# Performance work log

Hardware: AMD Instinct MI355X
Metric: run time of the kernel (lower is better)

Reference implementation:

```python
import jax, jax.numpy as jnp
import numpy as np

N = 100000      # nodes
E = 1600000     # edges
H = 128         # hidden_dim
L = 4           # num_layers (blocks AND inner GGC steps)
G = 512         # graphs in batch
IN = 128        # input_dim
OUT = 16        # output_dim
HS = H // 2     # mlp hidden


def setup_inputs() -> dict:
    key = jax.random.key(0)
    ks = jax.random.split(key, 24)
    s = 0.05
    inp = {
        "node_embed": jax.random.normal(ks[0], (N, IN), dtype=jnp.float32),
        "edge_index": jax.random.randint(ks[1], (2, E), 0, N, dtype=jnp.int32),
        "batch": jnp.sort(jax.random.randint(ks[2], (N,), 0, G, dtype=jnp.int32)),
        # nodeEmbed Linear
        "node_w": jax.random.normal(ks[3], (H, IN), dtype=jnp.float32) * s,
        "node_b": jnp.zeros((H,), dtype=jnp.float32),
        # per-block GatedGraphConv weights: [blocks, steps, H, H]
        "ggc_weight": jax.random.normal(ks[4], (L, L, H, H), dtype=jnp.float32) * s,
        # per-block GRUCell weights (torch layout: [3H, H], gates r,z,n)
        "gru_w_ih": jax.random.normal(ks[5], (L, 3 * H, H), dtype=jnp.float32) * s,
        "gru_w_hh": jax.random.normal(ks[6], (L, 3 * H, H), dtype=jnp.float32) * s,
        "gru_b_ih": jnp.zeros((L, 3 * H), dtype=jnp.float32),
        "gru_b_hh": jnp.zeros((L, 3 * H), dtype=jnp.float32),
        # cat_linear: H*L -> H
        "cat_w": jax.random.normal(ks[7], (H, H * L), dtype=jnp.float32) * s,
        "cat_b": jnp.zeros((H,), dtype=jnp.float32),
        # gate_nn: H -> 1
        "gate_w": jax.random.normal(ks[8], (1, H), dtype=jnp.float32) * s,
        "gate_b": jnp.zeros((1,), dtype=jnp.float32),
        # mlp
        "mlp_w1": jax.random.normal(ks[9], (HS, H), dtype=jnp.float32) * s,
        "mlp_b1": jnp.zeros((HS,), dtype=jnp.float32),
        "mlp_w2": jax.random.normal(ks[10], (HS, HS), dtype=jnp.float32) * s,
        "mlp_b2": jnp.zeros((HS,), dtype=jnp.float32),
        # heads
        "out_w": jax.random.normal(ks[11], (OUT, HS), dtype=jnp.float32) * s,
        "out_b": jnp.zeros((OUT,), dtype=jnp.float32),
        "line_w": jax.random.normal(ks[12], (OUT, H), dtype=jnp.float32) * s,
        "line_b": jnp.zeros((OUT,), dtype=jnp.float32),
    }
    return inp


def _gru_cell(m, h, w_ih, w_hh, b_ih, b_hh):
    gi = m @ w_ih.T + b_ih            # [N, 3H]
    gh = h @ w_hh.T + b_hh            # [N, 3H]
    i_r, i_z, i_n = jnp.split(gi, 3, axis=-1)
    h_r, h_z, h_n = jnp.split(gh, 3, axis=-1)
    r = jax.nn.sigmoid(i_r + h_r)
    z = jax.nn.sigmoid(i_z + h_z)
    n = jnp.tanh(i_n + r * h_n)
    return (1.0 - z) * n + z * h


def _gated_graph_conv(x, src, dst, W, w_ih, w_hh, b_ih, b_hh):
    n = x.shape[0]
    for i in range(W.shape[0]):       # fixed small step count
        m = x @ W[i]                  # [N, H]
        agg = jax.ops.segment_sum(m[src], dst, num_segments=n)  # scatter-add messages
        x = _gru_cell(agg, x, w_ih, w_hh, b_ih, b_hh)
    return x


def reference(node_embed, edge_index, batch, node_w, node_b, ggc_weight,
              gru_w_ih, gru_w_hh, gru_b_ih, gru_b_hh, cat_w, cat_b,
              gate_w, gate_b, mlp_w1, mlp_b1, mlp_w2, mlp_b2,
              out_w, out_b, line_w, line_b):
    src, dst = edge_index[0], edge_index[1]
    h0 = node_embed @ node_w.T + node_b                     # nodeEmbed
    # all residual blocks consume the SAME h0 (per original forward loop)
    outs = [
        _gated_graph_conv(h0, src, dst, ggc_weight[k], gru_w_ih[k],
                          gru_w_hh[k], gru_b_ih[k], gru_b_hh[k]) + h0
        for k in range(ggc_weight.shape[0])
    ]
    hidden = jnp.concatenate(outs, axis=-1) @ cat_w.T + cat_b  # [N, H]
    lineout = hidden @ line_w.T + line_b                       # [N, OUT]
    # attentional aggregation: scatter softmax over per-graph gates
    gate = (hidden @ gate_w.T + gate_b)[:, 0]                  # [N]
    gmax = jax.ops.segment_max(gate, batch, num_segments=G)
    ex = jnp.exp(gate - gmax[batch])
    denom = jax.ops.segment_sum(ex, batch, num_segments=G)
    alpha = ex / denom[batch]
    pooled = jax.ops.segment_sum(alpha[:, None] * hidden, batch, num_segments=G)  # [G, H]
    h = jax.nn.relu(pooled @ mlp_w1.T + mlp_b1)
    h = jax.nn.relu(h @ mlp_w2.T + mlp_b2)
    out = h @ out_w.T + out_b                                  # [G, OUT]
    return (out, lineout)
```

## Files before the change

kernel.cpp:

```cpp
#include <hip/hip_runtime.h>

#define N_NODES 100000
#define N_EDGES 1600000
#define HD 128
#define NH (N_NODES * HD)

typedef __attribute__((ext_vector_type(8))) short bf16x8;
typedef __attribute__((ext_vector_type(4))) float f32x4;

__device__ inline unsigned short f2bf(float f) {
  unsigned u = __float_as_uint(f);
  unsigned r = (u + 0x7FFFu + ((u >> 16) & 1u)) >> 16;
  return (unsigned short)r;
}
__device__ inline float bf2f(unsigned short b) {
  return __uint_as_float(((unsigned)b) << 16);
}
__device__ inline float sigm_f(float x) {
  return __builtin_amdgcn_rcpf(1.f + __expf(-x));
}
__device__ inline float tanh_f(float x) {
  return 1.f - 2.f * __builtin_amdgcn_rcpf(__expf(2.f * x) + 1.f);
}

__global__ __launch_bounds__(256) void gemm_h0_k(
    const float* __restrict__ A, const float* __restrict__ B,
    const float* __restrict__ bias, unsigned short* __restrict__ Cb, int M) {
  __shared__ float As[16][132];
  __shared__ float Bs[16][68];
  const int tid = threadIdx.x;
  const int row0 = blockIdx.x * 128;
  const int col0 = blockIdx.y * 64;
  const int tx = tid & 15, ty = tid >> 4;

  float acc[8][4];
#pragma unroll
  for (int i = 0; i < 8; i++)
#pragma unroll
    for (int j = 0; j < 4; j++) acc[i][j] = 0.f;

  const int lr = tid >> 2;
  const int kg = (tid & 3) * 4;

  for (int k0 = 0; k0 < 128; k0 += 16) {
#pragma unroll
    for (int h = 0; h < 2; ++h) {
      int r = lr + h * 64;
      float4 v = make_float4(0.f, 0.f, 0.f, 0.f);
      if (row0 + r < M)
        v = *reinterpret_cast<const float4*>(A + (size_t)(row0 + r) * 128 + k0 + kg);
      As[kg + 0][r] = v.x;
      As[kg + 1][r] = v.y;
      As[kg + 2][r] = v.z;
      As[kg + 3][r] = v.w;
    }
    {
      int c = lr;
      float4 v = *reinterpret_cast<const float4*>(B + (size_t)(col0 + c) * 128 + k0 + kg);
      Bs[kg + 0][c] = v.x;
      Bs[kg + 1][c] = v.y;
      Bs[kg + 2][c] = v.z;
      Bs[kg + 3][c] = v.w;
    }
    __syncthreads();
#pragma unroll
    for (int kk = 0; kk < 16; ++kk) {
      float a[8], b[4];
#pragma unroll
      for (int i = 0; i < 8; i++) a[i] = As[kk][ty * 8 + i];
#pragma unroll
      for (int j = 0; j < 4; j++) b[j] = Bs[kk][tx * 4 + j];
#pragma unroll
      for (int i = 0; i < 8; i++)
#pragma unroll
        for (int j = 0; j < 4; j++) acc[i][j] += a[i] * b[j];
    }
    __syncthreads();
  }

#pragma unroll
  for (int i = 0; i < 8; i++) {
    int r = row0 + ty * 8 + i;
    if (r < M) {
#pragma unroll
      for (int j = 0; j < 4; j++) {
        int c = col0 + tx * 4 + j;
        Cb[(size_t)r * 128 + c] = f2bf(acc[i][j] + bias[c]);
      }
    }
  }
}

__global__ __launch_bounds__(256) void gemm_wct_k(
    const float* __restrict__ w_ih, const float* __restrict__ ggc_w,
    float* __restrict__ Cout) {
  const int z = blockIdx.z;
  const float* A = w_ih + (size_t)(z >> 2) * 384 * 128;
  const float* B = ggc_w + (size_t)z * 128 * 128;
  float* C = Cout + (size_t)z * 384 * 128;
  __shared__ float As[16][132];
  __shared__ float Bs[16][68];
  const int tid = threadIdx.x;
  const int row0 = blockIdx.x * 128;
  const int col0 = blockIdx.y * 64;
  const int tx = tid & 15, ty = tid >> 4;

  float acc[8][4];
#pragma unroll
  for (int i = 0; i < 8; i++)
#pragma unroll
    for (int j = 0; j < 4; j++) acc[i][j] = 0.f;

  const int lr = tid >> 2;
  const int kg = (tid & 3) * 4;

  for (int k0 = 0; k0 < 128; k0 += 16) {
#pragma unroll
    for (int h = 0; h < 2; ++h) {
      int r = lr + h * 64;
      float4 v = *reinterpret_cast<const float4*>(A + (size_t)(row0 + r) * 128 + k0 + kg);
      As[kg + 0][r] = v.x;
      As[kg + 1][r] = v.y;
      As[kg + 2][r] = v.z;
      As[kg + 3][r] = v.w;
    }
    {
      int c = lr;
      float4 v = *reinterpret_cast<const float4*>(B + (size_t)(col0 + c) * 128 + k0 + kg);
      Bs[kg + 0][c] = v.x;
      Bs[kg + 1][c] = v.y;
      Bs[kg + 2][c] = v.z;
      Bs[kg + 3][c] = v.w;
    }
    __syncthreads();
#pragma unroll
    for (int kk = 0; kk < 16; ++kk) {
      float a[8], b[4];
#pragma unroll
      for (int i = 0; i < 8; i++) a[i] = As[kk][ty * 8 + i];
#pragma unroll
      for (int j = 0; j < 4; j++) b[j] = Bs[kk][tx * 4 + j];
#pragma unroll
      for (int i = 0; i < 8; i++)
#pragma unroll
        for (int j = 0; j < 4; j++) acc[i][j] += a[i] * b[j];
    }
    __syncthreads();
  }

#pragma unroll
  for (int i = 0; i < 8; i++) {
    int r = row0 + ty * 8 + i;
#pragma unroll
    for (int j = 0; j < 4; j++) {
      int c = col0 + tx * 4 + j;
      C[(size_t)r * 128 + c] = acc[i][j];
    }
  }
}

__global__ __launch_bounds__(256) void f2b_k(const float* __restrict__ a,
                                             unsigned short* __restrict__ b, int n) {
  int i = blockIdx.x * 256 + threadIdx.x;
  if (i * 4 >= n) return;
  float4 v = reinterpret_cast<const float4*>(a)[i];
  ushort4 o;
  o.x = f2bf(v.x);
  o.y = f2bf(v.y);
  o.z = f2bf(v.z);
  o.w = f2bf(v.w);
  reinterpret_cast<ushort4*>(b)[i] = o;
}

template <bool LAST>
__global__ __launch_bounds__(256) void gru_mfma4_k(
    const unsigned short* __restrict__ aggb,
    const unsigned short* __restrict__ xb_base, size_t xstride,
    const unsigned short* __restrict__ h0b,
    const unsigned short* __restrict__ wct_base, size_t wct_zs,
    const unsigned short* __restrict__ whh_base, size_t whh_zs,
    const float* __restrict__ bih_base, const float* __restrict__ bhh_base,
    unsigned short* __restrict__ xbout,
    int M, int nRowTiles) {
  const int z = blockIdx.z;
  const unsigned short* agg = aggb + (size_t)z * NH;
  const unsigned short* xb = xb_base + (size_t)z * xstride;
  unsigned short* out = xbout + (size_t)z * NH;
  const unsigned short* wctb = wct_base + (size_t)z * wct_zs;
  const unsigned short* whhb = whh_base + (size_t)z * whh_zs;
  const float* b_ih = bih_base + z * 384;
  const float* b_hh = bhh_base + z * 384;

  const int lane = threadIdx.x & 63;
  const int wave = threadIdx.x >> 6;
  const int lrow = lane & 15;
  const int kblk = lane >> 4;
  const int c = blockIdx.y * 16 + lrow;

  bf16x8 wf[6][4];
#pragma unroll
  for (int s = 0; s < 3; s++)
#pragma unroll
    for (int kk = 0; kk < 4; kk++) {
      size_t off = (size_t)(s * 128 + c) * 128 + kk * 32 + kblk * 8;
      wf[s][kk] = *reinterpret_cast<const bf16x8*>(wctb + off);
      wf[s + 3][kk] = *reinterpret_cast<const bf16x8*>(whhb + off);
    }
  const float bi0 = b_ih[c], bi1 = b_ih[128 + c], bi2 = b_ih[256 + c];
  const float bh0 = b_hh[c], bh1 = b_hh[128 + c], bh2 = b_hh[256 + c];

  const int tstride = gridDim.x * 4;
  for (int rt = blockIdx.x * 4 + wave; rt < nRowTiles; rt += tstride) {
    const int row0 = rt * 16;
    int arow = row0 + lrow;
    if (arow >= M) arow = M - 1;
    const size_t abase = (size_t)arow * 128 + kblk * 8;

    f32x4 acc[6];
#pragma unroll
    for (int s = 0; s < 6; s++) acc[s] = (f32x4)(0.f);
#pragma unroll
    for (int kk = 0; kk < 4; kk++) {
      bf16x8 a_ag = *reinterpret_cast<const bf16x8*>(agg + abase + kk * 32);
      bf16x8 a_x = *reinterpret_cast<const bf16x8*>(xb + abase + kk * 32);
      acc[0] = __builtin_amdgcn_mfma_f32_16x16x32_bf16(a_ag, wf[0][kk], acc[0], 0, 0, 0);
      acc[1] = __builtin_amdgcn_mfma_f32_16x16x32_bf16(a_ag, wf[1][kk], acc[1], 0, 0, 0);
      acc[2] = __builtin_amdgcn_mfma_f32_16x16x32_bf16(a_ag, wf[2][kk], acc[2], 0, 0, 0);
      acc[3] = __builtin_amdgcn_mfma_f32_16x16x32_bf16(a_x, wf[3][kk], acc[3], 0, 0, 0);
      acc[4] = __builtin_amdgcn_mfma_f32_16x16x32_bf16(a_x, wf[4][kk], acc[4], 0, 0, 0);
      acc[5] = __builtin_amdgcn_mfma_f32_16x16x32_bf16(a_x, wf[5][kk], acc[5], 0, 0, 0);
    }
#pragma unroll
    for (int r = 0; r < 4; r++) {
      int orow = row0 + kblk * 4 + r;
      if (orow >= M) continue;
      size_t idx = (size_t)orow * 128 + c;
      float ir = acc[0][r] + bi0;
      float iz = acc[1][r] + bi1;
      float in_ = acc[2][r] + bi2;
      float hr = acc[3][r] + bh0;
      float hz = acc[4][r] + bh1;
      float hn = acc[5][r] + bh2;
      float rg = sigm_f(ir + hr);
      float zg = sigm_f(iz + hz);
      float ng = tanh_f(in_ + rg * hn);
      float h = bf2f(xb[idx]);
      float nv = (1.f - zg) * ng + zg * h;
      if (LAST) nv += bf2f(h0b[idx]);
      out[idx] = f2bf(nv);
    }
  }
}

__global__ __launch_bounds__(256) void cat_mfma2_k(
    const unsigned short* __restrict__ outs,
    const unsigned short* __restrict__ wcatb,
    const float* __restrict__ cat_b, float* __restrict__ hidden, int M, int pair) {
  const int lane = threadIdx.x & 63;
  const int wave = threadIdx.x >> 6;
  const int row0 = blockIdx.x * 64 + wave * 16;
  const int c0 = blockIdx.y * 32;
  const int lrow = lane & 15;
  const int kb = lane >> 4;
  int arow = row0 + lrow;
  if (arow >= M) arow = M - 1;

  f32x4 acc[2];
  acc[0] = (f32x4)(0.f);
  acc[1] = (f32x4)(0.f);
#pragma unroll
  for (int kk = 0; kk < 8; kk++) {
    const unsigned short* ob = outs + (size_t)(kk >> 2) * NH;
    bf16x8 a = *reinterpret_cast<const bf16x8*>(
        ob + (size_t)arow * 128 + (kk & 3) * 32 + kb * 8);
#pragma unroll
    for (int t = 0; t < 2; t++) {
      bf16x8 b = *reinterpret_cast<const bf16x8*>(
          wcatb + (size_t)(c0 + t * 16 + lrow) * 512 + pair * 256 + (kk >> 2) * 128 +
          (kk & 3) * 32 + kb * 8);
      acc[t] = __builtin_amdgcn_mfma_f32_16x16x32_bf16(a, b, acc[t], 0, 0, 0);
    }
  }
#pragma unroll
  for (int r = 0; r < 4; r++) {
    int orow = row0 + kb * 4 + r;
    if (orow >= M) continue;
#pragma unroll
    for (int t = 0; t < 2; t++) {
      int c = c0 + t * 16 + lrow;
      size_t idx = (size_t)orow * 128 + c;
      float v = acc[t][r];
      v += (pair == 0) ? cat_b[c] : hidden[idx];
      hidden[idx] = v;
    }
  }
}

__global__ __launch_bounds__(256) void deg_hist_k(const int* __restrict__ dst,
                                                  int* __restrict__ deg) {
  int e = blockIdx.x * 256 + threadIdx.x;
  if (e >= N_EDGES) return;
  atomicAdd(&deg[dst[e]], 1);
}

__global__ __launch_bounds__(256) void scan1_k(const int* __restrict__ deg,
                                               int* __restrict__ offsets,
                                               int* __restrict__ bsum) {
  __shared__ int buf[256];
  int tid = threadIdx.x;
  int idx = blockIdx.x * 256 + tid;
  int v = (idx < N_NODES) ? deg[idx] : 0;
  buf[tid] = v;
  __syncthreads();
  for (int off = 1; off < 256; off <<= 1) {
    int t = (tid >= off) ? buf[tid - off] : 0;
    __syncthreads();
    buf[tid] += t;
    __syncthreads();
  }
  if (idx < N_NODES) offsets[idx] = buf[tid] - v;
  if (tid == 255) bsum[blockIdx.x] = buf[255];
}

__global__ __launch_bounds__(512) void scan2_k(int* __restrict__ bsum, int nb) {
  __shared__ int buf[512];
  int tid = threadIdx.x;
  int v = (tid < nb) ? bsum[tid] : 0;
  buf[tid] = v;
  __syncthreads();
  for (int off = 1; off < 512; off <<= 1) {
    int t = (tid >= off) ? buf[tid - off] : 0;
    __syncthreads();
    buf[tid] += t;
    __syncthreads();
  }
  if (tid < nb) bsum[tid] = buf[tid] - v;
}

__global__ __launch_bounds__(256) void scan3_k(int* __restrict__ offsets,
                                               const int* __restrict__ bsum) {
  int idx = blockIdx.x * 256 + threadIdx.x;
  if (idx < N_NODES) offsets[idx] += bsum[idx >> 8];
  if (idx == 0) offsets[N_NODES] = N_EDGES;
}

__global__ __launch_bounds__(256) void copy_int_k(const int* __restrict__ a,
                                                  int* __restrict__ b, int n) {
  int i = blockIdx.x * 256 + threadIdx.x;
  if (i < n) b[i] = a[i];
}

__global__ __launch_bounds__(256) void fill_k(const int* __restrict__ src,
                                              const int* __restrict__ dst,
                                              int* __restrict__ cursor,
                                              int* __restrict__ srcs_sorted) {
  int e = blockIdx.x * 256 + threadIdx.x;
  if (e >= N_EDGES) return;
  int pos = atomicAdd(&cursor[dst[e]], 1);
  srcs_sorted[pos] = src[e];
}

__global__ __launch_bounds__(256) void gather4_k(
    const unsigned short* __restrict__ xb_base, size_t xstride,
    const int* __restrict__ offsets, const int* __restrict__ srcs,
    unsigned short* __restrict__ aggb) {
  int wid = (blockIdx.x * 256 + threadIdx.x) >> 6;
  int lane = threadIdx.x & 63;
  if (wid >= 2 * N_NODES) return;
  int z = (wid >= N_NODES) ? 1 : 0;
  int node = wid - z * N_NODES;
  const unsigned short* xb = xb_base + (size_t)z * xstride;
  int beg = offsets[node], end = offsets[node + 1];
  int half = lane >> 5;
  int cg = (lane & 31) * 4;
  float a0 = 0.f, a1 = 0.f, a2 = 0.f, a3 = 0.f;
  int e = beg + half;
  for (; e + 2 < end; e += 4) {
    int s0 = srcs[e], s1 = srcs[e + 2];
    uint2 v0 = *reinterpret_cast<const uint2*>(xb + (size_t)s0 * 128 + cg);
    uint2 v1 = *reinterpret_cast<const uint2*>(xb + (size_t)s1 * 128 + cg);
    a0 += bf2f((unsigned short)(v0.x & 0xFFFFu));
    a1 += bf2f((unsigned short)(v0.x >> 16));
    a2 += bf2f((unsigned short)(v0.y & 0xFFFFu));
    a3 += bf2f((unsigned short)(v0.y >> 16));
    a0 += bf2f((unsigned short)(v1.x & 0xFFFFu));
    a1 += bf2f((unsigned short)(v1.x >> 16));
    a2 += bf2f((unsigned short)(v1.y & 0xFFFFu));
    a3 += bf2f((unsigned short)(v1.y >> 16));
  }
  if (e < end) {
    int s0 = srcs[e];
    uint2 v0 = *reinterpret_cast<const uint2*>(xb + (size_t)s0 * 128 + cg);
    a0 += bf2f((unsigned short)(v0.x & 0xFFFFu));
    a1 += bf2f((unsigned short)(v0.x >> 16));
    a2 += bf2f((unsigned short)(v0.y & 0xFFFFu));
    a3 += bf2f((unsigned short)(v0.y >> 16));
  }
  a0 += __shfl_down(a0, 32);
  a1 += __shfl_down(a1, 32);
  a2 += __shfl_down(a2, 32);
  a3 += __shfl_down(a3, 32);
  if (half == 0) {
    uint2 o;
    o.x = (unsigned)f2bf(a0) | ((unsigned)f2bf(a1) << 16);
    o.y = (unsigned)f2bf(a2) | ((unsigned)f2bf(a3) << 16);
    *reinterpret_cast<uint2*>(aggb + (size_t)z * NH + (size_t)node * 128 + cg) = o;
  }
}

__global__ __launch_bounds__(256) void lineout_k(
    const float* __restrict__ hidden, const float* __restrict__ W,
    const float* __restrict__ b, float* __restrict__ out) {
  __shared__ float Ws[16 * 128];
  for (int i = threadIdx.x; i < 2048; i += 256) Ws[i] = W[i];
  __syncthreads();
  int r = threadIdx.x >> 4, c = threadIdx.x & 15;
  int n = blockIdx.x * 16 + r;
  if (n >= N_NODES) return;
  const float* h = hidden + (size_t)n * 128;
  const float* w = Ws + c * 128;
  float acc = 0.f;
#pragma unroll 8
  for (int k = 0; k < 128; k++) acc += h[k] * w[k];
  out[(size_t)n * 16 + c] = acc + b[c];
}

__global__ __launch_bounds__(256) void gate_k(
    const float* __restrict__ hidden, const float* __restrict__ gw,
    const float* __restrict__ gb, float* __restrict__ gate) {
  int wid = (blockIdx.x * 256 + threadIdx.x) >> 6;
  int lane = threadIdx.x & 63;
  if (wid >= N_NODES) return;
  const float* h = hidden + (size_t)wid * 128;
  float s = h[lane] * gw[lane] + h[64 + lane] * gw[64 + lane];
#pragma unroll
  for (int off = 32; off; off >>= 1) s += __shfl_down(s, off);
  if (lane == 0) gate[wid] = s + gb[0];
}

__global__ void graph_start_k(const int* __restrict__ batch, int* __restrict__ gs) {
  int g = threadIdx.x;
  if (g > 512) return;
  if (g == 512) {
    gs[512] = N_NODES;
    return;
  }
  int lo = 0, hi = N_NODES;
  while (lo < hi) {
    int mid = (lo + hi) >> 1;
    if (batch[mid] < g) lo = mid + 1;
    else hi = mid;
  }
  gs[g] = lo;
}

__global__ __launch_bounds__(256) void pool_fused_k(
    const float* __restrict__ hidden, const float* __restrict__ gate,
    const int* __restrict__ gs, float* __restrict__ ex,
    float* __restrict__ pooled) {
  const int g = blockIdx.x;
  const int beg = gs[g], end = gs[g + 1];
  const int tid = threadIdx.x, lane = tid & 63, wv = tid >> 6;
  __shared__ float red[4];
  __shared__ float sval;
  __shared__ float colbuf[256];

  if (end <= beg) {
    if (tid < 128) pooled[(size_t)g * 128 + tid] = 0.f;
    return;
  }
  float m = -3.4e38f;
  for (int n = beg + tid; n < end; n += 256) m = fmaxf(m, gate[n]);
#pragma unroll
  for (int off = 32; off; off >>= 1) m = fmaxf(m, __shfl_down(m, off));
  if (lane == 0) red[wv] = m;
  __syncthreads();
  if (tid == 0) sval = fmaxf(fmaxf(red[0], red[1]), fmaxf(red[2], red[3]));
  __syncthreads();
  const float mx = sval;
  float s = 0.f;
  for (int n = beg + tid; n < end; n += 256) {
    float e = __expf(gate[n] - mx);
    ex[n] = e;
    s += e;
  }
#pragma unroll
  for (int off = 32; off; off >>= 1) s += __shfl_down(s, off);
  if (lane == 0) red[wv] = s;
  __syncthreads();
  if (tid == 0) sval = red[0] + red[1] + red[2] + red[3];
  __syncthreads();
  const float denom = sval;
  const int col = tid & 127, half = tid >> 7;
  float acc = 0.f;
  for (int n = beg + half; n < end; n += 2)
    acc += ex[n] * hidden[(size_t)n * 128 + col];
  colbuf[tid] = acc;
  __syncthreads();
  if (tid < 128)
    pooled[(size_t)g * 128 + tid] = (colbuf[tid] + colbuf[tid + 128]) / denom;
}

__global__ void mlp1_k(const float* __restrict__ pooled, const float* __restrict__ w,
                       const float* __restrict__ b, float* __restrict__ h1) {
  int g = blockIdx.x, j = threadIdx.x;
  const float* p = pooled + (size_t)g * 128;
  const float* wr = w + (size_t)j * 128;
  float acc = 0.f;
#pragma unroll 8
  for (int k = 0; k < 128; k++) acc += p[k] * wr[k];
  acc += b[j];
  h1[g * 64 + j] = acc > 0.f ? acc : 0.f;
}

__global__ void mlp2_k(const float* __restrict__ h1, const float* __restrict__ w,
                       const float* __restrict__ b, float* __restrict__ h2) {
  int g = blockIdx.x, j = threadIdx.x;
  const float* p = h1 + (size_t)g * 64;
  const float* wr = w + (size_t)j * 64;
  float acc = 0.f;
#pragma unroll 8
  for (int k = 0; k < 64; k++) acc += p[k] * wr[k];
  acc += b[j];
  h2[g * 64 + j] = acc > 0.f ? acc : 0.f;
}

__global__ void outhead_k(const float* __restrict__ h2, const float* __restrict__ w,
                          const float* __restrict__ b, float* __restrict__ out) {
  int g = blockIdx.x, j = threadIdx.x;
  if (j >= 16) return;
  const float* p = h2 + (size_t)g * 64;
  const float* wr = w + (size_t)j * 64;
  float acc = 0.f;
#pragma unroll 8
  for (int k = 0; k < 64; k++) acc += p[k] * wr[k];
  out[g * 16 + j] = acc + b[j];
}

extern "C" void kernel_launch(void* const* d_in, const int* in_sizes, int n_in,
                              void* d_out, int out_size, void* d_ws, size_t ws_size,
                              hipStream_t stream) {
  const float* node_embed = (const float*)d_in[0];
  const int* eidx = (const int*)d_in[1];
  const int* batch = (const int*)d_in[2];
  const float* node_w = (const float*)d_in[3];
  const float* node_b = (const float*)d_in[4];
  const float* ggc_w = (const float*)d_in[5];
  const float* w_ih = (const float*)d_in[6];
  const float* w_hh = (const float*)d_in[7];
  const float* b_ih = (const float*)d_in[8];
  const float* b_hh = (const float*)d_in[9];
  const float* cat_w = (const float*)d_in[10];
  const float* cat_b = (const float*)d_in[11];
  const float* gate_w = (const float*)d_in[12];
  const float* gate_b = (const float*)d_in[13];
  const float* mlp_w1 = (const float*)d_in[14];
  const float* mlp_b1 = (const float*)d_in[15];
  const float* mlp_w2 = (const float*)d_in[16];
  const float* mlp_b2 = (const float*)d_in[17];
  const float* out_w = (const float*)d_in[18];
  const float* out_b = (const float*)d_in[19];
  const float* line_w = (const float*)d_in[20];
  const float* line_b = (const float*)d_in[21];

  const int* src = eidx;
  const int* dst = eidx + N_EDGES;

  float* hidden = (float*)d_ws;
  unsigned short* h0b = (unsigned short*)(hidden + (size_t)NH);
  unsigned short* X0 = h0b + (size_t)NH;
  unsigned short* X1 = X0 + (size_t)2 * NH;
  unsigned short* aggb = X1 + (size_t)2 * NH;
  unsigned short* wctb = aggb + (size_t)2 * NH;
  unsigned short* whhb = wctb + 16 * 384 * 128;
  unsigned short* wcatb = whhb + 4 * 384 * 128;
  int* offsets = (int*)(wcatb + 128 * 512);
  int* cursor = offsets + N_NODES + 1;
  int* srcs_sorted = cursor + N_NODES;
  int* bsum = srcs_sorted + N_EDGES;
  int* gs = bsum + 512;
  float* WcTf = (float*)aggb;

  float* out_graph = (float*)d_out;
  float* out_line = (float*)d_out + 512 * 16;

  dim3 blk(256);
  const int gM128 = (N_NODES + 127) / 128;
  const int gM64 = (N_NODES + 63) / 64;
  const int gE = (N_EDGES + 255) / 256;
  const int nScanBlk = (N_NODES + 255) / 256;
  const int nRowTiles = (N_NODES + 15) / 16;
  const size_t S = (size_t)384 * 128;

  hipMemsetAsync(cursor, 0, N_NODES * sizeof(int), stream);
  deg_hist_k<<<gE, blk, 0, stream>>>(dst, cursor);
  scan1_k<<<nScanBlk, blk, 0, stream>>>(cursor, offsets, bsum);
  scan2_k<<<1, 512, 0, stream>>>(bsum, nScanBlk);
  scan3_k<<<nScanBlk, blk, 0, stream>>>(offsets, bsum);
  copy_int_k<<<(N_NODES + 255) / 256, blk, 0, stream>>>(offsets, cursor, N_NODES);
  fill_k<<<gE, blk, 0, stream>>>(src, dst, cursor, srcs_sorted);
  graph_start_k<<<1, 576, 0, stream>>>(batch, gs);

  gemm_wct_k<<<dim3(3, 2, 16), blk, 0, stream>>>(w_ih, ggc_w, WcTf);
  f2b_k<<<(16 * 384 * 128 / 4 + 255) / 256, blk, 0, stream>>>(WcTf, wctb, 16 * 384 * 128);
  f2b_k<<<(4 * 384 * 128 / 4 + 255) / 256, blk, 0, stream>>>(w_hh, whhb, 4 * 384 * 128);
  f2b_k<<<(128 * 512 / 4 + 255) / 256, blk, 0, stream>>>(cat_w, wcatb, 128 * 512);

  gemm_h0_k<<<dim3(gM128, 2), blk, 0, stream>>>(node_embed, node_w, node_b, h0b, N_NODES);

  const int gGather = (2 * N_NODES * 64 + 255) / 256;
  const dim3 gruGrid(200, 8, 2);
  for (int p = 0; p < 2; p++) {
    const float* bih_p = b_ih + (size_t)p * 2 * 384;
    const float* bhh_p = b_hh + (size_t)p * 2 * 384;
    const unsigned short* whh_p = whhb + (size_t)p * 2 * S;
    for (int i = 0; i < 4; i++) {
      const unsigned short* wct_pi = wctb + ((size_t)8 * p + i) * S;
      const unsigned short* xin;
      size_t xs;
      unsigned short* xout;
      if (i == 0) { xin = h0b; xs = 0; xout = X0; }
      else if (i == 1) { xin = X0; xs = NH; xout = X1; }
      else if (i == 2) { xin = X1; xs = NH; xout = X0; }
      else { xin = X0; xs = NH; xout = X1; }
      gather4_k<<<gGather, blk, 0, stream>>>(xin, xs, offsets, srcs_sorted, aggb);
      if (i < 3)
        gru_mfma4_k<false><<<gruGrid, blk, 0, stream>>>(
            aggb, xin, xs, h0b, wct_pi, 4 * S, whh_p, S, bih_p, bhh_p, xout,
            N_NODES, nRowTiles);
      else
        gru_mfma4_k<true><<<gruGrid, blk, 0, stream>>>(
            aggb, xin, xs, h0b, wct_pi, 4 * S, whh_p, S, bih_p, bhh_p, xout,
            N_NODES, nRowTiles);
    }
    cat_mfma2_k<<<dim3(gM64, 4), blk, 0, stream>>>(X1, wcatb, cat_b, hidden, N_NODES, p);
  }

  lineout_k<<<(N_NODES + 15) / 16, blk, 0, stream>>>(hidden, line_w, line_b, out_line);

  float* gate = (float*)X0;
  float* ex = (float*)X0 + N_NODES;
  float* pooled = (float*)aggb;
  float* h1 = pooled + 512 * 128;
  float* h2 = h1 + 512 * 64;

  gate_k<<<(N_NODES * 64 + 255) / 256, blk, 0, stream>>>(hidden, gate_w, gate_b, gate);
  pool_fused_k<<<512, blk, 0, stream>>>(hidden, gate, gs, ex, pooled);
  mlp1_k<<<512, 64, 0, stream>>>(pooled, mlp_w1, mlp_b1, h1);
  mlp2_k<<<512, 64, 0, stream>>>(h1, mlp_w2, mlp_b2, h2);
  outhead_k<<<512, 64, 0, stream>>>(h2, out_w, out_b, out_graph);
}
```

Baseline: 2.845 ms.

## Dedupe first-step gather, deepen gather unroll, prefetch GRU epilogue loads, widen grid

At the first GGC step both blocks of a pair read the same h0, so the gather now runs for one block only and both GRU blocks read that single aggregate through a zero z-stride. The gather loop is unrolled to four neighbours per half-wave to keep more loads in flight. The GRU kernel loads the h and h0 epilogue values before the MFMA loop, drops row bounds checks because N is divisible by 16, and doubles the grid x dimension. This removes redundant gather traffic and exposes load latency to overlap, at the cost of relying on N being a multiple of 16.

```diff
diff --git a/kernel.cpp b/kernel.cpp
--- a/kernel.cpp
+++ b/kernel.cpp
@@ -173,17 +173,16 @@
 }
 
 template <bool LAST>
-__global__ __launch_bounds__(256) void gru_mfma4_k(
-    const unsigned short* __restrict__ aggb,
+__global__ __launch_bounds__(256) void gru_mfma5_k(
+    const unsigned short* __restrict__ agg_base, size_t agg_zs,
     const unsigned short* __restrict__ xb_base, size_t xstride,
     const unsigned short* __restrict__ h0b,
     const unsigned short* __restrict__ wct_base, size_t wct_zs,
     const unsigned short* __restrict__ whh_base, size_t whh_zs,
     const float* __restrict__ bih_base, const float* __restrict__ bhh_base,
-    unsigned short* __restrict__ xbout,
-    int M, int nRowTiles) {
+    unsigned short* __restrict__ xbout, int nRowTiles) {
   const int z = blockIdx.z;
-  const unsigned short* agg = aggb + (size_t)z * NH;
+  const unsigned short* agg = agg_base + (size_t)z * agg_zs;
   const unsigned short* xb = xb_base + (size_t)z * xstride;
   unsigned short* out = xbout + (size_t)z * NH;
   const unsigned short* wctb = wct_base + (size_t)z * wct_zs;
@@ -212,9 +211,15 @@
   const int tstride = gridDim.x * 4;
   for (int rt = blockIdx.x * 4 + wave; rt < nRowTiles; rt += tstride) {
     const int row0 = rt * 16;
-    int arow = row0 + lrow;
-    if (arow >= M) arow = M - 1;
-    const size_t abase = (size_t)arow * 128 + kblk * 8;
+    const size_t abase = (size_t)(row0 + lrow) * 128 + kblk * 8;
+    const int ob = row0 + kblk * 4;
+
+    unsigned short hxv[4], h0v[4];
+#pragma unroll
+    for (int r = 0; r < 4; r++) {
+      hxv[r] = xb[(size_t)(ob + r) * 128 + c];
+      if (LAST) h0v[r] = h0b[(size_t)(ob + r) * 128 + c];
+    }
 
     f32x4 acc[6];
 #pragma unroll
@@ -232,9 +237,7 @@
     }
 #pragma unroll
     for (int r = 0; r < 4; r++) {
-      int orow = row0 + kblk * 4 + r;
-      if (orow >= M) continue;
-      size_t idx = (size_t)orow * 128 + c;
+      size_t idx = (size_t)(ob + r) * 128 + c;
       float ir = acc[0][r] + bi0;
       float iz = acc[1][r] + bi1;
       float in_ = acc[2][r] + bi2;
@@ -244,17 +247,16 @@
       float rg = sigm_f(ir + hr);
       float zg = sigm_f(iz + hz);
       float ng = tanh_f(in_ + rg * hn);
-      float h = bf2f(xb[idx]);
+      float h = bf2f(hxv[r]);
       float nv = (1.f - zg) * ng + zg * h;
-      if (LAST) nv += bf2f(h0b[idx]);
+      if (LAST) nv += bf2f(h0v[r]);
       out[idx] = f2bf(nv);
     }
   }
 }
 
 __global__ __launch_bounds__(256) void cat_mfma2_k(
-    const unsigned short* __restrict__ outs,
-    const unsigned short* __restrict__ wcatb,
+    const unsigned short* __restrict__ outs, const unsigned short* __restrict__ wcatb,
     const float* __restrict__ cat_b, float* __restrict__ hidden, int M, int pair) {
   const int lane = threadIdx.x & 63;
   const int wave = threadIdx.x >> 6;
@@ -360,13 +362,13 @@
   srcs_sorted[pos] = src[e];
 }
 
-__global__ __launch_bounds__(256) void gather4_k(
+__global__ __launch_bounds__(256) void gather5_k(
     const unsigned short* __restrict__ xb_base, size_t xstride,
     const int* __restrict__ offsets, const int* __restrict__ srcs,
-    unsigned short* __restrict__ aggb) {
+    unsigned short* __restrict__ aggb, int nz) {
   int wid = (blockIdx.x * 256 + threadIdx.x) >> 6;
   int lane = threadIdx.x & 63;
-  if (wid >= 2 * N_NODES) return;
+  if (wid >= nz * N_NODES) return;
   int z = (wid >= N_NODES) ? 1 : 0;
   int node = wid - z * N_NODES;
   const unsigned short* xb = xb_base + (size_t)z * xstride;
@@ -375,20 +377,22 @@
   int cg = (lane & 31) * 4;
   float a0 = 0.f, a1 = 0.f, a2 = 0.f, a3 = 0.f;
   int e = beg + half;
-  for (; e + 2 < end; e += 4) {
-    int s0 = srcs[e], s1 = srcs[e + 2];
+  for (; e + 6 < end; e += 8) {
+    int s0 = srcs[e], s1 = srcs[e + 2], s2 = srcs[e + 4], s3 = srcs[e + 6];
     uint2 v0 = *reinterpret_cast<const uint2*>(xb + (size_t)s0 * 128 + cg);
     uint2 v1 = *reinterpret_cast<const uint2*>(xb + (size_t)s1 * 128 + cg);
-    a0 += bf2f((unsigned short)(v0.x & 0xFFFFu));
-    a1 += bf2f((unsigned short)(v0.x >> 16));
-    a2 += bf2f((unsigned short)(v0.y & 0xFFFFu));
-    a3 += bf2f((unsigned short)(v0.y >> 16));
-    a0 += bf2f((unsigned short)(v1.x & 0xFFFFu));
-    a1 += bf2f((unsigned short)(v1.x >> 16));
-    a2 += bf2f((unsigned short)(v1.y & 0xFFFFu));
-    a3 += bf2f((unsigned short)(v1.y >> 16));
-  }
-  if (e < end) {
+    uint2 v2 = *reinterpret_cast<const uint2*>(xb + (size_t)s2 * 128 + cg);
+    uint2 v3 = *reinterpret_cast<const uint2*>(xb + (size_t)s3 * 128 + cg);
+    a0 += bf2f((unsigned short)(v0.x & 0xFFFFu)) + bf2f((unsigned short)(v1.x & 0xFFFFu)) +
+          bf2f((unsigned short)(v2.x & 0xFFFFu)) + bf2f((unsigned short)(v3.x & 0xFFFFu));
+    a1 += bf2f((unsigned short)(v0.x >> 16)) + bf2f((unsigned short)(v1.x >> 16)) +
+          bf2f((unsigned short)(v2.x >> 16)) + bf2f((unsigned short)(v3.x >> 16));
+    a2 += bf2f((unsigned short)(v0.y & 0xFFFFu)) + bf2f((unsigned short)(v1.y & 0xFFFFu)) +
+          bf2f((unsigned short)(v2.y & 0xFFFFu)) + bf2f((unsigned short)(v3.y & 0xFFFFu));
+    a3 += bf2f((unsigned short)(v0.y >> 16)) + bf2f((unsigned short)(v1.y >> 16)) +
+          bf2f((unsigned short)(v2.y >> 16)) + bf2f((unsigned short)(v3.y >> 16));
+  }
+  for (; e < end; e += 2) {
     int s0 = srcs[e];
     uint2 v0 = *reinterpret_cast<const uint2*>(xb + (size_t)s0 * 128 + cg);
     a0 += bf2f((unsigned short)(v0.x & 0xFFFFu));
@@ -589,7 +593,7 @@
   const int gM64 = (N_NODES + 63) / 64;
   const int gE = (N_EDGES + 255) / 256;
   const int nScanBlk = (N_NODES + 255) / 256;
-  const int nRowTiles = (N_NODES + 15) / 16;
+  const int nRowTiles = N_NODES / 16;
   const size_t S = (size_t)384 * 128;
 
   hipMemsetAsync(cursor, 0, N_NODES * sizeof(int), stream);
@@ -608,8 +612,9 @@
 
   gemm_h0_k<<<dim3(gM128, 2), blk, 0, stream>>>(node_embed, node_w, node_b, h0b, N_NODES);
 
-  const int gGather = (2 * N_NODES * 64 + 255) / 256;
-  const dim3 gruGrid(200, 8, 2);
+  const int gGather2 = (2 * N_NODES * 64 + 255) / 256;
+  const int gGather1 = (N_NODES * 64 + 255) / 256;
+  const dim3 gruGrid(400, 8, 2);
   for (int p = 0; p < 2; p++) {
     const float* bih_p = b_ih + (size_t)p * 2 * 384;
     const float* bhh_p = b_hh + (size_t)p * 2 * 384;
@@ -623,15 +628,17 @@
       else if (i == 1) { xin = X0; xs = NH; xout = X1; }
       else if (i == 2) { xin = X1; xs = NH; xout = X0; }
       else { xin = X0; xs = NH; xout = X1; }
-      gather4_k<<<gGather, blk, 0, stream>>>(xin, xs, offsets, srcs_sorted, aggb);
+      const size_t agg_zs = (i == 0) ? 0 : (size_t)NH;
+      gather5_k<<<(i == 0 ? gGather1 : gGather2), blk, 0, stream>>>(
+          xin, xs, offsets, srcs_sorted, aggb, (i == 0 ? 1 : 2));
       if (i < 3)
-        gru_mfma4_k<false><<<gruGrid, blk, 0, stream>>>(
-            aggb, xin, xs, h0b, wct_pi, 4 * S, whh_p, S, bih_p, bhh_p, xout,
-            N_NODES, nRowTiles);
+        gru_mfma5_k<false><<<gruGrid, blk, 0, stream>>>(
+            aggb, agg_zs, xin, xs, h0b, wct_pi, 4 * S, whh_p, S, bih_p, bhh_p,
+            xout, nRowTiles);
       else
-        gru_mfma4_k<true><<<gruGrid, blk, 0, stream>>>(
-            aggb, xin, xs, h0b, wct_pi, 4 * S, whh_p, S, bih_p, bhh_p, xout,
-            N_NODES, nRowTiles);
+        gru_mfma5_k<true><<<gruGrid, blk, 0, stream>>>(
+            aggb, agg_zs, xin, xs, h0b, wct_pi, 4 * S, whh_p, S, bih_p, bhh_p,
+            xout, nRowTiles);
     }
     cat_mfma2_k<<<dim3(gM64, 4), blk, 0, stream>>>(X1, wcatb, cat_b, hidden, N_NODES, p);
   }
```

Result: no change. 2.796 ms (-1.7%).
